# Performance work log

Hardware: AMD Instinct MI355X
Metric: run time of the kernel (lower is better)

Reference implementation:

```python
import jax, jax.numpy as jnp
import numpy as np

D_MODEL = 2048
N_HEADS = 16
D_HEAD = 128
BATCH = 2
SEQ = 2048
INIT_STD = 0.02
N_LAYERS = 12


def setup_inputs() -> dict:
    key = jax.random.key(0)
    ks = jax.random.split(key, 5)
    attn_std = INIT_STD
    proj_std = INIT_STD / np.sqrt(2 * N_LAYERS)
    return {
        "normalized_resid_pre": jax.random.normal(ks[0], (BATCH, SEQ, D_MODEL), jnp.float32),
        "W_Q": jax.random.normal(ks[1], (N_HEADS, D_MODEL, D_HEAD), jnp.float32) * attn_std,
        "W_K": jax.random.normal(ks[2], (N_HEADS, D_MODEL, D_HEAD), jnp.float32) * attn_std,
        "W_V": jax.random.normal(ks[3], (N_HEADS, D_MODEL, D_HEAD), jnp.float32) * attn_std,
        "W_O": jax.random.normal(ks[4], (N_HEADS, D_HEAD, D_MODEL), jnp.float32) * proj_std,
        "b_Q": jnp.zeros((N_HEADS, D_HEAD), jnp.float32),
        "b_K": jnp.zeros((N_HEADS, D_HEAD), jnp.float32),
        "b_V": jnp.zeros((N_HEADS, D_HEAD), jnp.float32),
        "b_O": jnp.zeros((D_MODEL,), jnp.float32),
    }


def reference(normalized_resid_pre, W_Q, W_K, W_V, W_O, b_Q, b_K, b_V, b_O):
    x = normalized_resid_pre
    # q,k,v: [batch, posn, nheads, d_head]
    q = jnp.einsum('bsd,hde->bshe', x, W_Q) + b_Q
    k = jnp.einsum('bsd,hde->bshe', x, W_K) + b_K
    v = jnp.einsum('bsd,hde->bshe', x, W_V) + b_V
    # scores: [batch, nheads, posn_Q, posn_K]
    scores = jnp.einsum('bqhe,bkhe->bhqk', q, k) / jnp.sqrt(jnp.float32(D_HEAD))
    S = scores.shape[-1]
    causal = jnp.tril(jnp.ones((S, S), bool))
    scores = jnp.where(causal, scores, jnp.float32(-jnp.inf))
    pattern = jax.nn.softmax(scores, axis=-1)
    z = jnp.einsum('bhqk,bkhe->bqhe', pattern, v)
    attn_out = jnp.einsum('bqhe,hed->bqd', z, W_O) + b_O
    return attn_out
```

## Files before the change

### kernel.cpp

```cpp
#include <hip/hip_runtime.h>
#include <hip/hip_bf16.h>

typedef __hip_bfloat16 bf16;
typedef __attribute__((ext_vector_type(8))) short bf16x8;
typedef __attribute__((ext_vector_type(4))) short bf16x4;
typedef __attribute__((ext_vector_type(4))) float f32x4;

#define D_MODEL 2048
#define SEQ     2048
#define NH      16
#define DH      128
#define BATCH   2
#define MTOT    (BATCH*SEQ)

__device__ __forceinline__ void async_cp16(const bf16* g, bf16* l) {
    __builtin_amdgcn_global_load_lds(
        (const __attribute__((address_space(1))) void*)g,
        (__attribute__((address_space(3))) void*)l, 16, 0, 0);
}

__device__ __forceinline__ short bf16bits(float f) {
    bf16 b = __float2bfloat16(f);
    return *reinterpret_cast<short*>(&b);
}

__global__ __launch_bounds__(256) void cvt_k(const float* __restrict__ in,
                                             bf16* __restrict__ out) {
    const long i = ((long)blockIdx.x * 256 + threadIdx.x) * 8;
    float4 a = *(const float4*)(in + i);
    float4 b = *(const float4*)(in + i + 4);
    __align__(16) bf16 t[8];
    t[0] = __float2bfloat16(a.x); t[1] = __float2bfloat16(a.y);
    t[2] = __float2bfloat16(a.z); t[3] = __float2bfloat16(a.w);
    t[4] = __float2bfloat16(b.x); t[5] = __float2bfloat16(b.y);
    t[6] = __float2bfloat16(b.z); t[7] = __float2bfloat16(b.w);
    *(bf16x8*)(out + i) = *(const bf16x8*)t;
}

__global__ __launch_bounds__(256) void transpose_cvt3_k(
    const float* __restrict__ in0, const float* __restrict__ in1,
    const float* __restrict__ in2,
    bf16* __restrict__ out, int R, int Cn, int mats_per_src)
{
    __shared__ float t[32][33];
    const int z = blockIdx.z;
    const int src = z / mats_per_src, mat = z % mats_per_src;
    const float* in = (src == 0) ? in0 : (src == 1) ? in1 : in2;
    const float* inm = in + (long)mat * R * Cn;
    bf16* outm = out + (long)z * R * Cn;
    const int c0 = blockIdx.x * 32, r0 = blockIdx.y * 32;
    const int tx = threadIdx.x & 31, ty = threadIdx.x >> 5;
#pragma unroll
    for (int i = 0; i < 4; ++i)
        t[ty + i*8][tx] = inm[(long)(r0 + ty + i*8) * Cn + c0 + tx];
    __syncthreads();
#pragma unroll
    for (int i = 0; i < 4; ++i)
        outm[(long)(c0 + ty + i*8) * R + r0 + tx] = __float2bfloat16(t[tx][ty + i*8]);
}

__global__ __launch_bounds__(256) void transpose_v_k(
    const bf16* __restrict__ V, bf16* __restrict__ VT)
{
    __shared__ bf16 t[32][33];
    const int bh = blockIdx.z;
    const int b = bh >> 4, h = bh & 15;
    const bf16* inm = V + (long)b*SEQ*D_MODEL + h*DH;
    bf16* outm = VT + (long)bh*DH*SEQ;
    const int r0 = blockIdx.x * 32;
    const int c0 = blockIdx.y * 32;
    const int tx = threadIdx.x & 31, ty = threadIdx.x >> 5;
#pragma unroll
    for (int i = 0; i < 4; ++i)
        t[ty + i*8][tx] = inm[(long)(r0 + ty + i*8)*D_MODEL + c0 + tx];
    __syncthreads();
#pragma unroll
    for (int i = 0; i < 4; ++i)
        outm[(long)(c0 + ty + i*8)*SEQ + r0 + tx] = t[tx][ty + i*8];
}

template <bool C_F32>
__device__ __forceinline__ void gemm128x128(
    const bf16* __restrict__ A, int lda,
    const bf16* __restrict__ Bt, int ldb,
    void* __restrict__ C, int ldc,
    const float* __restrict__ bias,
    int Kdim, int m0, int n0)
{
    __shared__ __align__(16) bf16 As[128*32];
    __shared__ __align__(16) bf16 Bs[128*32];
    const int tid  = threadIdx.x;
    const int wave = tid >> 6, lane = tid & 63;
    const int lr = lane & 15, lq = lane >> 4;
    const int wrow = wave >> 1, wcol = wave & 1;
    const int sr = lane >> 2, sk = (lane & 3) * 8;

    const f32x4 zero4 = {0.f, 0.f, 0.f, 0.f};
    f32x4 acc[4][4];
#pragma unroll
    for (int i = 0; i < 4; ++i)
#pragma unroll
        for (int j = 0; j < 4; ++j) acc[i][j] = zero4;

    for (int k0 = 0; k0 < Kdim; k0 += 32) {
#pragma unroll
        for (int c = 0; c < 2; ++c) {
            const int r = wave*32 + c*16;
            async_cp16(A  + (long)(m0 + r + sr)*lda + k0 + sk, As + r*32);
            async_cp16(Bt + (long)(n0 + r + sr)*ldb + k0 + sk, Bs + r*32);
        }
        __syncthreads();
        bf16x8 af[4], bfr[4];
#pragma unroll
        for (int i = 0; i < 4; ++i)
            af[i] = *(const bf16x8*)(As + (wrow*64 + i*16 + lr)*32 + lq*8);
#pragma unroll
        for (int j = 0; j < 4; ++j)
            bfr[j] = *(const bf16x8*)(Bs + (wcol*64 + j*16 + lr)*32 + lq*8);
#pragma unroll
        for (int i = 0; i < 4; ++i)
#pragma unroll
            for (int j = 0; j < 4; ++j)
                acc[i][j] = __builtin_amdgcn_mfma_f32_16x16x32_bf16(af[i], bfr[j], acc[i][j], 0, 0, 0);
        __syncthreads();
    }
#pragma unroll
    for (int j = 0; j < 4; ++j) {
        const int col = n0 + wcol*64 + j*16 + lr;
        const float bv = bias[col];
#pragma unroll
        for (int i = 0; i < 4; ++i) {
            const int row = m0 + wrow*64 + i*16 + lq*4;
#pragma unroll
            for (int r = 0; r < 4; ++r) {
                const float v = acc[i][j][r] + bv;
                if constexpr (C_F32) ((float*)C)[(long)(row + r)*ldc + col] = v;
                else ((bf16*)C)[(long)(row + r)*ldc + col] = __float2bfloat16(v);
            }
        }
    }
}

__global__ __launch_bounds__(256) void qkv_gemm_k(
    const bf16* __restrict__ X, const bf16* __restrict__ WT3,
    const float* __restrict__ bQ, const float* __restrict__ bK, const float* __restrict__ bV,
    bf16* __restrict__ Qo, bf16* __restrict__ Ko, bf16* __restrict__ Vo)
{
    const int mt  = blockIdx.x;
    const int sel = blockIdx.y >> 4;
    const int h   = blockIdx.y & 15;
    const float* bias; bf16* C;
    if (sel == 0)      { bias = bQ; C = Qo; }
    else if (sel == 1) { bias = bK; C = Ko; }
    else               { bias = bV; C = Vo; }
    gemm128x128<false>(X, D_MODEL, WT3 + (long)blockIdx.y*DH*D_MODEL, D_MODEL,
                       C + h*DH, NH*DH, bias + h*DH, D_MODEL, mt*128, 0);
}

__global__ __launch_bounds__(256) void out_gemm_k(
    const bf16* __restrict__ Z, const bf16* __restrict__ WOT,
    const float* __restrict__ bO, float* __restrict__ Out)
{
    gemm128x128<true>(Z, D_MODEL, WOT, D_MODEL, Out, D_MODEL, bO, D_MODEL,
                      (int)blockIdx.x*128, (int)blockIdx.y*128);
}

__global__ __launch_bounds__(256) void flash_k(
    const bf16* __restrict__ Q, const bf16* __restrict__ K,
    const bf16* __restrict__ VT, bf16* __restrict__ Z)
{
    __shared__ __align__(16) bf16 Ks[4*64*32];
    __shared__ __align__(16) bf16 Vts[2*128*32];
    __shared__ __align__(16) bf16 Ps[64*72];

    const int qt = (int)(gridDim.x - 1) - (int)blockIdx.x;
    const int bh = blockIdx.y;
    const int b  = bh >> 4, h = bh & 15;
    const long base = (long)b*SEQ*D_MODEL + h*DH;
    const bf16* Qb  = Q + base;
    const bf16* Kb  = K + base;
    const bf16* VTb = VT + (long)bh*DH*SEQ;
    bf16* Zb = Z + base;
    const int q0 = qt*64;
    const int tid = threadIdx.x, wave = tid >> 6, lane = tid & 63;
    const int lr = lane & 15, lq = lane >> 4;

    bf16x8 aq[4];
#pragma unroll
    for (int ks = 0; ks < 4; ++ks)
        aq[ks] = *(const bf16x8*)(Qb + (long)(q0 + wave*16 + lr)*D_MODEL + ks*32 + lq*8);

    const f32x4 zero4 = {0.f, 0.f, 0.f, 0.f};
    f32x4 o_acc[8];
#pragma unroll
    for (int jf = 0; jf < 8; ++jf) o_acc[jf] = zero4;
    float m_run = -1e30f, l_run = 0.f;

    const float scale = 0.08838834764831845f;

    for (int kt = 0; kt <= qt; ++kt) {
        const int k0 = kt*64;
        __syncthreads();
#pragma unroll
        for (int c = 0; c < 4; ++c)
            async_cp16(Kb + (long)(k0 + c*16 + (lane>>2))*D_MODEL + wave*32 + (lane&3)*8,
                       Ks + wave*2048 + c*512);
#pragma unroll
        for (int kf = 0; kf < 2; ++kf)
#pragma unroll
            for (int i = 0; i < 2; ++i)
                async_cp16(VTb + (long)(wave*32 + i*16 + (lane>>2))*SEQ + k0 + kf*32 + (lane&3)*8,
                           Vts + kf*4096 + (wave*32 + i*16)*32);
        __syncthreads();

        f32x4 sc[4];
#pragma unroll
        for (int mt = 0; mt < 4; ++mt) sc[mt] = zero4;
#pragma unroll
        for (int mt = 0; mt < 4; ++mt)
#pragma unroll
            for (int ks = 0; ks < 4; ++ks) {
                bf16x8 bk = *(const bf16x8*)(Ks + ks*2048 + (mt*16 + lr)*32 + lq*8);
                sc[mt] = __builtin_amdgcn_mfma_f32_16x16x32_bf16(bk, aq[ks], sc[mt], 0, 0, 0);
            }

        if (kt == qt) {
            const int qrl = wave*16 + lr;
#pragma unroll
            for (int mt = 0; mt < 4; ++mt)
#pragma unroll
                for (int r = 0; r < 4; ++r)
                    if (mt*16 + lq*4 + r > qrl) sc[mt][r] = -1e30f;
        }

        float mx = sc[0][0];
#pragma unroll
        for (int mt = 0; mt < 4; ++mt)
#pragma unroll
            for (int r = 0; r < 4; ++r) mx = fmaxf(mx, sc[mt][r]);
        mx = fmaxf(mx, __shfl_xor(mx, 16, 64));
        mx = fmaxf(mx, __shfl_xor(mx, 32, 64));
        mx *= scale;

        const float mn = fmaxf(m_run, mx);
        const float al = __expf(m_run - mn);
        float rs = 0.f;
#pragma unroll
        for (int mt = 0; mt < 4; ++mt)
#pragma unroll
            for (int r = 0; r < 4; ++r) {
                const float p = __expf(fmaf(sc[mt][r], scale, -mn));
                sc[mt][r] = p;
                rs += p;
            }
        rs += __shfl_xor(rs, 16, 64);
        rs += __shfl_xor(rs, 32, 64);
        l_run = l_run * al + rs;
        m_run = mn;
#pragma unroll
        for (int jf = 0; jf < 8; ++jf)
#pragma unroll
            for (int r = 0; r < 4; ++r) o_acc[jf][r] *= al;

#pragma unroll
        for (int mt = 0; mt < 4; ++mt)
#pragma unroll
            for (int r = 0; r < 4; ++r)
                Ps[(wave*16 + lr)*72 + mt*16 + lq*4 + r] = __float2bfloat16(sc[mt][r]);

        bf16x8 pb0 = *(const bf16x8*)(Ps + (wave*16 + lr)*72 + lq*8);
        bf16x8 pb1 = *(const bf16x8*)(Ps + (wave*16 + lr)*72 + 32 + lq*8);

#pragma unroll
        for (int jf = 0; jf < 8; ++jf) {
            bf16x8 av0 = *(const bf16x8*)(Vts + (jf*16 + lr)*32 + lq*8);
            bf16x8 av1 = *(const bf16x8*)(Vts + 4096 + (jf*16 + lr)*32 + lq*8);
            o_acc[jf] = __builtin_amdgcn_mfma_f32_16x16x32_bf16(av0, pb0, o_acc[jf], 0, 0, 0);
            o_acc[jf] = __builtin_amdgcn_mfma_f32_16x16x32_bf16(av1, pb1, o_acc[jf], 0, 0, 0);
        }
    }

    const float inv = 1.f / l_run;
    const long zrow = (long)(q0 + wave*16 + lr) * D_MODEL;
#pragma unroll
    for (int jf = 0; jf < 8; ++jf) {
        bf16x4 pk;
#pragma unroll
        for (int r = 0; r < 4; ++r) pk[r] = bf16bits(o_acc[jf][r] * inv);
        *(bf16x4*)(Zb + zrow + jf*16 + lq*4) = pk;
    }
}

extern "C" void kernel_launch(void* const* d_in, const int* in_sizes, int n_in,
                              void* d_out, int out_size, void* d_ws, size_t ws_size,
                              hipStream_t stream) {
    const float* X  = (const float*)d_in[0];
    const float* WQ = (const float*)d_in[1];
    const float* WK = (const float*)d_in[2];
    const float* WV = (const float*)d_in[3];
    const float* WO = (const float*)d_in[4];
    const float* bQ = (const float*)d_in[5];
    const float* bK = (const float*)d_in[6];
    const float* bV = (const float*)d_in[7];
    const float* bO = (const float*)d_in[8];
    float* out = (float*)d_out;

    bf16* ws = (bf16*)d_ws;
    const long WSZ = (long)NH*DH*D_MODEL;
    const long MSZ = (long)MTOT*D_MODEL;
    bf16* Xb  = ws;
    bf16* WT3 = Xb + MSZ;
    bf16* WOT = WT3 + 3*WSZ;
    bf16* Qb  = WOT + WSZ;
    bf16* Kb  = Qb + MSZ;
    bf16* Vb  = Kb + MSZ;
    bf16* Zb  = Xb;
    bf16* VT  = WT3;

    cvt_k<<<MSZ/(256*8), 256, 0, stream>>>(X, Xb);
    transpose_cvt3_k<<<dim3(DH/32, D_MODEL/32, 3*NH), 256, 0, stream>>>(
        WQ, WK, WV, WT3, D_MODEL, DH, NH);
    transpose_cvt3_k<<<dim3(D_MODEL/32, D_MODEL/32, 1), 256, 0, stream>>>(
        WO, WO, WO, WOT, D_MODEL, D_MODEL, 1);

    qkv_gemm_k<<<dim3(MTOT/128, 48), 256, 0, stream>>>(Xb, WT3, bQ, bK, bV, Qb, Kb, Vb);
    transpose_v_k<<<dim3(SEQ/32, DH/32, BATCH*NH), 256, 0, stream>>>(Vb, VT);
    flash_k<<<dim3(SEQ/64, BATCH*NH), 256, 0, stream>>>(Qb, Kb, VT, Zb);
    out_gemm_k<<<dim3(MTOT/128, D_MODEL/128), 256, 0, stream>>>(Zb, WOT, bO, out);
}
```

Measured before the change: 459.2 us.

## Swizzle K/V tiles in LDS, add lazy softmax rescale and MFMA priority

Changes the LDS layout of the K and V^T tiles to full-row, XOR-swizzled storage so async global loads cover longer contiguous segments and MFMA operand reads avoid bank conflicts. It also adds a lazy online-softmax rescale that skips the O accumulator rescaling unless the running max grows by more than a threshold. P is now packed into vector bf16x4 stores, and s_setprio is raised around the MFMA loops. The lazy rescale lets exponent values grow up to e^8 before renormalising, which slightly changes numerics.

```diff
diff --git a/kernel.cpp b/kernel.cpp
--- a/kernel.cpp
+++ b/kernel.cpp
@@ -169,8 +169,8 @@
     const bf16* __restrict__ Q, const bf16* __restrict__ K,
     const bf16* __restrict__ VT, bf16* __restrict__ Z)
 {
-    __shared__ __align__(16) bf16 Ks[4*64*32];
-    __shared__ __align__(16) bf16 Vts[2*128*32];
+    __shared__ __align__(16) bf16 Ks[64*128];
+    __shared__ __align__(16) bf16 Vts[128*64];
     __shared__ __align__(16) bf16 Ps[64*72];
 
     const int qt = (int)(gridDim.x - 1) - (int)blockIdx.x;
@@ -184,6 +184,12 @@
     const int q0 = qt*64;
     const int tid = threadIdx.x, wave = tid >> 6, lane = tid & 63;
     const int lr = lane & 15, lq = lane >> 4;
+    const int rx = lr & 7;
+
+    const int ks_key_off = lane >> 4;
+    const int ks_slot    = lane & 15;
+    const int vt_row_off = lane >> 3;
+    const int vt_slot    = lane & 7;
 
     bf16x8 aq[4];
 #pragma unroll
@@ -202,27 +208,31 @@
         const int k0 = kt*64;
         __syncthreads();
 #pragma unroll
-        for (int c = 0; c < 4; ++c)
-            async_cp16(Kb + (long)(k0 + c*16 + (lane>>2))*D_MODEL + wave*32 + (lane&3)*8,
-                       Ks + wave*2048 + c*512);
-#pragma unroll
-        for (int kf = 0; kf < 2; ++kf)
-#pragma unroll
-            for (int i = 0; i < 2; ++i)
-                async_cp16(VTb + (long)(wave*32 + i*16 + (lane>>2))*SEQ + k0 + kf*32 + (lane&3)*8,
-                           Vts + kf*4096 + (wave*32 + i*16)*32);
+        for (int c = 0; c < 4; ++c) {
+            const int key = (wave*4 + c)*4 + ks_key_off;
+            async_cp16(Kb + (long)(k0 + key)*D_MODEL + ((ks_slot ^ (key & 7)) * 8),
+                       Ks + (wave*4 + c)*512);
+        }
+#pragma unroll
+        for (int c = 0; c < 4; ++c) {
+            const int f = (wave*4 + c)*8 + vt_row_off;
+            async_cp16(VTb + (long)f*SEQ + k0 + ((vt_slot ^ (f & 7)) * 8),
+                       Vts + (wave*4 + c)*512);
+        }
         __syncthreads();
 
         f32x4 sc[4];
 #pragma unroll
         for (int mt = 0; mt < 4; ++mt) sc[mt] = zero4;
+        __builtin_amdgcn_s_setprio(1);
 #pragma unroll
         for (int mt = 0; mt < 4; ++mt)
 #pragma unroll
             for (int ks = 0; ks < 4; ++ks) {
-                bf16x8 bk = *(const bf16x8*)(Ks + ks*2048 + (mt*16 + lr)*32 + lq*8);
+                bf16x8 bk = *(const bf16x8*)(Ks + (mt*16 + lr)*128 + (((ks*4 + lq) ^ rx) * 8));
                 sc[mt] = __builtin_amdgcn_mfma_f32_16x16x32_bf16(bk, aq[ks], sc[mt], 0, 0, 0);
             }
+        __builtin_amdgcn_s_setprio(0);
 
         if (kt == qt) {
             const int qrl = wave*16 + lr;
@@ -242,42 +252,51 @@
         mx = fmaxf(mx, __shfl_xor(mx, 32, 64));
         mx *= scale;
 
-        const float mn = fmaxf(m_run, mx);
-        const float al = __expf(m_run - mn);
+        if (!__all(mx - m_run <= 8.0f)) {
+            const float mn = fmaxf(m_run, mx);
+            const float al = __expf(m_run - mn);
+            l_run *= al;
+#pragma unroll
+            for (int jf = 0; jf < 8; ++jf)
+#pragma unroll
+                for (int r = 0; r < 4; ++r) o_acc[jf][r] *= al;
+            m_run = mn;
+        }
+
         float rs = 0.f;
 #pragma unroll
         for (int mt = 0; mt < 4; ++mt)
 #pragma unroll
             for (int r = 0; r < 4; ++r) {
-                const float p = __expf(fmaf(sc[mt][r], scale, -mn));
+                const float p = __expf(fmaf(sc[mt][r], scale, -m_run));
                 sc[mt][r] = p;
                 rs += p;
             }
         rs += __shfl_xor(rs, 16, 64);
         rs += __shfl_xor(rs, 32, 64);
-        l_run = l_run * al + rs;
-        m_run = mn;
-#pragma unroll
-        for (int jf = 0; jf < 8; ++jf)
-#pragma unroll
-            for (int r = 0; r < 4; ++r) o_acc[jf][r] *= al;
-
-#pragma unroll
-        for (int mt = 0; mt < 4; ++mt)
-#pragma unroll
-            for (int r = 0; r < 4; ++r)
-                Ps[(wave*16 + lr)*72 + mt*16 + lq*4 + r] = __float2bfloat16(sc[mt][r]);
+        l_run += rs;
+
+#pragma unroll
+        for (int mt = 0; mt < 4; ++mt) {
+            bf16x4 pk;
+#pragma unroll
+            for (int r = 0; r < 4; ++r) pk[r] = bf16bits(sc[mt][r]);
+            *(bf16x4*)(Ps + (wave*16 + lr)*72 + mt*16 + lq*4) = pk;
+        }
 
         bf16x8 pb0 = *(const bf16x8*)(Ps + (wave*16 + lr)*72 + lq*8);
         bf16x8 pb1 = *(const bf16x8*)(Ps + (wave*16 + lr)*72 + 32 + lq*8);
 
+        __builtin_amdgcn_s_setprio(1);
 #pragma unroll
         for (int jf = 0; jf < 8; ++jf) {
-            bf16x8 av0 = *(const bf16x8*)(Vts + (jf*16 + lr)*32 + lq*8);
-            bf16x8 av1 = *(const bf16x8*)(Vts + 4096 + (jf*16 + lr)*32 + lq*8);
+            const int f = jf*16 + lr;
+            bf16x8 av0 = *(const bf16x8*)(Vts + f*64 + ((lq ^ rx) * 8));
+            bf16x8 av1 = *(const bf16x8*)(Vts + f*64 + (((4 + lq) ^ rx) * 8));
             o_acc[jf] = __builtin_amdgcn_mfma_f32_16x16x32_bf16(av0, pb0, o_acc[jf], 0, 0, 0);
             o_acc[jf] = __builtin_amdgcn_mfma_f32_16x16x32_bf16(av1, pb1, o_acc[jf], 0, 0, 0);
         }
+        __builtin_amdgcn_s_setprio(0);
     }
 
     const float inv = 1.f / l_run;
```

Result: no change. 450.6 us (-1.9%).
